# Kernel tuning notes

Hardware: AMD Instinct MI355X
Metric: run time of the kernel (lower is better)

The kernel has to match this reference:

```python
import jax, jax.numpy as jnp
import numpy as np
import math

N_HEADS = 8

def _head_dirs():
    # 8 trigrams = corners of {-1,+1}^3, L2-normalized -> each row / sqrt(3)
    t = np.array([[ (i >> 2 & 1) * 2 - 1, (i >> 1 & 1) * 2 - 1, (i & 1) * 2 - 1]
                  for i in range(8)], dtype=np.float32)
    return jnp.asarray(t / np.sqrt(3.0, dtype=np.float32))

def setup_inputs() -> dict:
    key = jax.random.key(0)
    k1, k2, k3, k4 = jax.random.split(key, 4)
    B, T, C = 2, 2048, 1024
    x = jax.random.normal(k1, (B, T, C), dtype=jnp.float32)
    w_qkv = jax.random.normal(k2, (C, 3 * C), dtype=jnp.float32) * (1.0 / math.sqrt(C))
    w_out = jax.random.normal(k3, (C, C), dtype=jnp.float32) * (1.0 / math.sqrt(C))
    head_scales = jax.random.normal(k4, (N_HEADS,), dtype=jnp.float32) * 0.1
    return {"x": x, "w_qkv": w_qkv, "w_out": w_out, "head_scales": head_scales}

def reference(x, w_qkv, w_out, head_scales):
    B, T, C = x.shape
    H = N_HEADS
    hd = C // H
    scale = 1.0 / math.sqrt(hd)
    dirs = _head_dirs()  # [H,3], fixed buffer

    qkv = (x @ w_qkv).reshape(B, T, 3, H, hd)
    q = jnp.transpose(qkv[:, :, 0], (0, 2, 1, 3))  # [B,H,T,hd]
    k = jnp.transpose(qkv[:, :, 1], (0, 2, 1, 3))
    v = jnp.transpose(qkv[:, :, 2], (0, 2, 1, 3))

    scores = jnp.einsum('bhqd,bhkd->bhqk', q, k) * scale  # [B,H,T,T]
    causal = jnp.tril(jnp.ones((T, T), dtype=bool))
    scores = jnp.where(causal[None, None], scores, -jnp.inf)

    # rank-1 geometric (trigram) bias on first 3 dims of q,k
    q_proj = jnp.einsum('bhtd,hd->bht', q[..., :3], dirs)  # [B,H,T]
    k_proj = jnp.einsum('bhtd,hd->bht', k[..., :3], dirs)
    geo = q_proj[..., :, None] * k_proj[..., None, :]       # [B,H,T,T]
    scores = scores + head_scales[None, :, None, None] * geo

    attn = jax.nn.softmax(scores, axis=-1)
    out = jnp.einsum('bhqk,bhkd->bqhd', attn, v).reshape(B, T, C)
    return out @ w_out
```

## Files before the change

kernel.cpp:

```cpp
#include <hip/hip_runtime.h>
#include <hip/hip_bf16.h>
#include <cstdint>
#include <cstddef>


namespace {
constexpr int kB = 2, kT = 2048, kC = 1024, kHD = 128;
constexpr int kM = kB * kT;
constexpr int kN3 = 3 * kC;
constexpr float kScale = 0.08838834764831845f;
constexpr float kInvS3 = 0.57735026918962576f;
constexpr float kL2E  = 1.4426950408889634f;
}

typedef __bf16 bf16x8 __attribute__((ext_vector_type(8)));
typedef float f32x4 __attribute__((ext_vector_type(4)));
typedef unsigned short u16x8 __attribute__((ext_vector_type(8)));
typedef unsigned short u16x4 __attribute__((ext_vector_type(4)));
typedef unsigned int u32x4 __attribute__((ext_vector_type(4)));

__device__ __forceinline__ unsigned short f2b(float f) {
  return __builtin_bit_cast(unsigned short, (__bf16)f);
}
__device__ __forceinline__ float b2f(unsigned short u) {
  return (float)__builtin_bit_cast(__bf16, u);
}
__device__ __forceinline__ void gll16(const void* g, void* lds) {
  __builtin_amdgcn_global_load_lds(
      (const __attribute__((address_space(1))) unsigned int*)g,
      (__attribute__((address_space(3))) unsigned int*)lds, 16, 0, 0);
}
__device__ __forceinline__ bf16x8 ldsv(const unsigned short* p) {
  return __builtin_bit_cast(bf16x8, *(const u16x8*)p);
}
__device__ __forceinline__ uint2 tr16(const unsigned short* p) {
  uint2 r;
  unsigned off = (unsigned)(uintptr_t)(const __attribute__((address_space(3))) unsigned short*)p;
  asm volatile("ds_read_b64_tr_b16 %0, %1" : "=v"(r) : "v"(off));
  return r;
}

__device__ __forceinline__ void tc_body(const float* __restrict__ in,
                                        unsigned short* __restrict__ out,
                                        int R, int Cin, int bx, int by, int t) {
  __shared__ float tile[64][65];
  const int r0 = by * 64, c0 = bx * 64;
  const int tr = t >> 4, tc4 = (t & 15) * 4;
#pragma unroll
  for (int rr = 0; rr < 4; ++rr) {
    int r = tr + rr * 16;
    float4 v = *(const float4*)&in[(size_t)(r0 + r) * Cin + c0 + tc4];
    tile[r][tc4 + 0] = v.x; tile[r][tc4 + 1] = v.y;
    tile[r][tc4 + 2] = v.z; tile[r][tc4 + 3] = v.w;
  }
  __syncthreads();
#pragma unroll
  for (int rr = 0; rr < 4; ++rr) {
    int c = tr + rr * 16;
    u16x4 o = { f2b(tile[tc4 + 0][c]), f2b(tile[tc4 + 1][c]),
                f2b(tile[tc4 + 2][c]), f2b(tile[tc4 + 3][c]) };
    *(u16x4*)&out[(size_t)(c0 + c) * R + r0 + tc4] = o;
  }
}

__global__ void k_prep(const float* __restrict__ x, unsigned short* __restrict__ xb,
                       const float* __restrict__ wqkv, unsigned short* __restrict__ wqkvT) {
  const int bid = (int)blockIdx.x;
  const int t = threadIdx.x;
  if (bid < 4096) {
    int i = bid * 256 + t;
    float4 v = ((const float4*)x)[i];
    u16x4 o = { f2b(v.x), f2b(v.y), f2b(v.z), f2b(v.w) };
    ((u16x4*)xb)[i] = o;
  } else {
    int r = bid - 4096;
    tc_body(wqkv, wqkvT, kC, kN3, r % 48, r / 48, t);
  }
}

__global__ __launch_bounds__(256, 2) void k_gemm(
    const unsigned short* __restrict__ A,
    const unsigned short* __restrict__ Bt,
    unsigned short* __restrict__ Cb,
    float* __restrict__ Cf,
    int M, int N, int K, int ldc) {
  __shared__ unsigned short sA[2][4096];
  __shared__ unsigned short sB[2][4096];
  const int t = threadIdx.x;
  const int lane = t & 63, wave = t >> 6;
  const int g = lane >> 4, c16 = lane & 15;
  const int wr = wave >> 1, wc = wave & 1;
  const int brow = blockIdx.x * 128, bcol = blockIdx.y * 128;
  const int NT = K >> 5;

  f32x4 acc[4][4];
#pragma unroll
  for (int m = 0; m < 4; ++m)
#pragma unroll
    for (int n = 0; n < 4; ++n) acc[m][n] = 0.f;

  auto stage = [&](int buf, int kt) {
    const int k0 = kt * 32;
#pragma unroll
    for (int is = 0; is < 2; ++is) {
      int row = is * 64 + (t >> 2);
      int gs = (t & 3) ^ (row & 3);
      gll16(&A[(size_t)(brow + row) * K + k0 + gs * 8], &sA[buf][is * 2048 + wave * 512]);
      gll16(&Bt[(size_t)(bcol + row) * K + k0 + gs * 8], &sB[buf][is * 2048 + wave * 512]);
    }
  };

  stage(0, 0);
  __syncthreads();
  for (int kt = 0; kt < NT; ++kt) {
    if (kt + 1 < NT) stage((kt + 1) & 1, kt + 1);
    const int buf = kt & 1;
    bf16x8 av[4], bv[4];
#pragma unroll
    for (int m = 0; m < 4; ++m) {
      int row = wr * 64 + m * 16 + c16;
      av[m] = ldsv(&sA[buf][row * 32 + (g ^ (row & 3)) * 8]);
    }
#pragma unroll
    for (int n = 0; n < 4; ++n) {
      int row = wc * 64 + n * 16 + c16;
      bv[n] = ldsv(&sB[buf][row * 32 + (g ^ (row & 3)) * 8]);
    }
    __builtin_amdgcn_s_setprio(1);
#pragma unroll
    for (int m = 0; m < 4; ++m)
#pragma unroll
      for (int n = 0; n < 4; ++n)
        acc[m][n] = __builtin_amdgcn_mfma_f32_16x16x32_bf16(av[m], bv[n], acc[m][n], 0, 0, 0);
    __builtin_amdgcn_s_setprio(0);
    __syncthreads();
  }

  const int orow = brow + wr * 64, ocol = bcol + wc * 64;
  if (Cb != nullptr) {
#pragma unroll
    for (int m = 0; m < 4; ++m)
#pragma unroll
      for (int n = 0; n < 4; ++n)
#pragma unroll
        for (int jj = 0; jj < 4; ++jj)
          Cb[(size_t)(orow + m * 16 + g * 4 + jj) * ldc + ocol + n * 16 + c16] =
              f2b(acc[m][n][jj]);
  } else {
#pragma unroll
    for (int m = 0; m < 4; ++m)
#pragma unroll
      for (int n = 0; n < 4; ++n)
#pragma unroll
        for (int jj = 0; jj < 4; ++jj)
          Cf[(size_t)(orow + m * 16 + g * 4 + jj) * ldc + ocol + n * 16 + c16] =
              acc[m][n][jj];
  }
}

__constant__ unsigned char kItem[44] = {
  60, 61,
  62, 56, 57, 58, 52,
  53, 54, 48, 49,
  50, 44, 45, 46, 40,
  41, 42, 36, 37,
  38, 32, 33, 34, 28,
  29, 30, 24, 25,
  26, 20, 21, 22, 16,
  17, 18, 12, 13, 8, 9,
  14, 4, 5, 0 };

__global__ __launch_bounds__(256, 2) void k_attn(
    const unsigned short* __restrict__ qkv,
    const float* __restrict__ head_scales,
    unsigned short* __restrict__ pO0,
    unsigned short* __restrict__ pO1,
    unsigned short* __restrict__ pO2,
    float2* __restrict__ pml) {
  __shared__ unsigned short sK[8192];
  __shared__ unsigned short sV[2][8192];
  __shared__ float sKp[2][64];

  const int t = threadIdx.x;
  const int lane = t & 63, wave = t >> 6;
  const int g = lane >> 4, c16 = lane & 15;
  const int bh = blockIdx.x;
  const int it = kItem[blockIdx.y];
  const int qt = it >> 2, c = it & 3;
  const int n = 2 * qt + 2;
  const int nc = (qt == 0) ? 1 : (qt <= 2) ? 2 : 3;
  const int cbase = n / nc, crem = n % nc;
  const int t0 = c * cbase + (c < crem ? c : crem);
  const int t1 = t0 + cbase + (c < crem ? 1 : 0);

  const int b = bh >> 3, h = bh & 7;
  const float hs = head_scales[h];
  const float sx = (h & 4) ? 1.f : -1.f;
  const float sy = (h & 2) ? 1.f : -1.f;
  const float sz = (h & 1) ? 1.f : -1.f;

  const int q0w = qt * 128 + wave * 32;
  const size_t rowbase = (size_t)b * kT;

  bf16x8 aq[2][4];
  float qp[2];
#pragma unroll
  for (int m = 0; m < 2; ++m) {
    const unsigned short* qrow = &qkv[(rowbase + q0w + m * 16 + c16) * kN3 + h * kHD];
#pragma unroll
    for (int ks = 0; ks < 4; ++ks) aq[m][ks] = ldsv(qrow + ks * 32 + g * 8);
    qp[m] = hs * kInvS3 * (sx * b2f(qrow[0]) + sy * b2f(qrow[1]) + sz * b2f(qrow[2]));
  }

  float mrow[2] = { -__builtin_inff(), -__builtin_inff() };
  float lrow[2] = { 0.f, 0.f };
  f32x4 oacc[2][8];
#pragma unroll
  for (int m = 0; m < 2; ++m)
#pragma unroll
    for (int dn = 0; dn < 8; ++dn) oacc[m][dn] = 0.f;

  uint2 kpr;

  auto stageK = [&](int jt) {
    const int j0 = jt * 64;
#pragma unroll
    for (int is = 0; is < 4; ++is) {
      int row = is * 16 + (t >> 4);
      int gp = t & 15;
      int gs = (gp & 8) | ((gp ^ (row & 7)) & 7);
      gll16(&qkv[(rowbase + j0 + row) * kN3 + kC + h * kHD + gs * 8],
            &sK[is * 2048 + wave * 512]);
    }
  };
  auto stageV = [&](int jt, int buf) {
    const int j0 = jt * 64;
    const int vrow = ((lane >> 3) << 2) + ((lane >> 1) & 3);
    const int vcol = (lane & 1) * 8;
#pragma unroll
    for (int d = 0; d < 2; ++d) {
      const int dn = wave * 2 + d;
#pragma unroll
      for (int hf2 = 0; hf2 < 2; ++hf2) {
        gll16(&qkv[(rowbase + j0 + hf2 * 32 + vrow) * kN3 + 2 * kC + h * kHD
                   + dn * 16 + vcol],
              &sV[buf][dn * 1024 + hf2 * 512]);
      }
    }
  };
  auto loadKp = [&](int jt) {
    if (wave == 0)
      kpr = *(const uint2*)&qkv[(rowbase + jt * 64 + lane) * kN3 + kC + h * kHD];
  };
  auto writeKp = [&](int buf) {
    if (wave == 0) {
      float e0 = b2f((unsigned short)(kpr.x & 0xffffu));
      float e1 = b2f((unsigned short)(kpr.x >> 16));
      float e2 = b2f((unsigned short)(kpr.y & 0xffffu));
      sKp[buf][lane] = kInvS3 * (sx * e0 + sy * e1 + sz * e2);
    }
  };

  stageK(t0); stageV(t0, 0); loadKp(t0);
  writeKp(0);
  __syncthreads();

  for (int jt = t0; jt < t1; ++jt) {
    const int vbuf = (jt - t0) & 1;
    const bool more = (jt + 1 < t1);
    const int j0 = jt * 64;

    f32x4 s[2][4];
#pragma unroll
    for (int m = 0; m < 2; ++m)
#pragma unroll
      for (int nn = 0; nn < 4; ++nn) s[m][nn] = 0.f;
#pragma unroll
    for (int ks = 0; ks < 4; ++ks) {
      bf16x8 kb[4];
#pragma unroll
      for (int nn = 0; nn < 4; ++nn) {
        int gp = ks * 4 + g;
        int gp2 = (gp & 8) | ((gp ^ (c16 & 7)) & 7);
        kb[nn] = ldsv(&sK[(nn * 16 + c16) * 128 + gp2 * 8]);
      }
      __builtin_amdgcn_s_setprio(1);
#pragma unroll
      for (int m = 0; m < 2; ++m)
#pragma unroll
        for (int nn = 0; nn < 4; ++nn)
          s[m][nn] = __builtin_amdgcn_mfma_f32_16x16x32_bf16(kb[nn], aq[m][ks], s[m][nn], 0, 0, 0);
      __builtin_amdgcn_s_setprio(0);
    }

    __syncthreads();
    if (more) { stageK(jt + 1); stageV(jt + 1, vbuf ^ 1); loadKp(jt + 1); }

    float kpv[4][4];
#pragma unroll
    for (int nn = 0; nn < 4; ++nn)
#pragma unroll
      for (int jj = 0; jj < 4; ++jj) kpv[nn][jj] = sKp[vbuf][nn * 16 + g * 4 + jj];

    const bool edge = (jt >= 2 * qt);
    unsigned int paf[2][2][4];
#pragma unroll
    for (int m = 0; m < 2; ++m) {
      const int qg = q0w + m * 16 + c16;
      float vmax = -__builtin_inff();
#pragma unroll
      for (int nn = 0; nn < 4; ++nn)
#pragma unroll
        for (int jj = 0; jj < 4; ++jj) {
          float xv = s[m][nn][jj] * kScale + qp[m] * kpv[nn][jj];
          if (edge) {
            int kvg = j0 + nn * 16 + g * 4 + jj;
            xv = (kvg <= qg) ? xv : -__builtin_inff();
          }
          s[m][nn][jj] = xv;
          vmax = fmaxf(vmax, xv);
        }
      vmax = fmaxf(vmax, __shfl_xor(vmax, 16, 64));
      vmax = fmaxf(vmax, __shfl_xor(vmax, 32, 64));

      if (__any(vmax > mrow[m] + 8.f)) {
        float mnew = fmaxf(mrow[m], vmax);
        float mc0 = fmaxf(mnew, -1e30f);
        float alpha = exp2f((mrow[m] - mc0) * kL2E);
        mrow[m] = mnew;
        lrow[m] *= alpha;
        float ao[4];
#pragma unroll
        for (int jj = 0; jj < 4; ++jj)
          ao[jj] = __shfl(alpha, (lane & 48) | (g * 4 + jj), 64);
#pragma unroll
        for (int dn = 0; dn < 8; ++dn)
#pragma unroll
          for (int jj = 0; jj < 4; ++jj) oacc[m][dn][jj] *= ao[jj];
      }

      unsigned int pk[4][2];
      {
        const float mc = fmaxf(mrow[m], -1e30f);
        float ls = 0.f;
#pragma unroll
        for (int nn = 0; nn < 4; ++nn) {
          float p0 = exp2f((s[m][nn][0] - mc) * kL2E);
          float p1 = exp2f((s[m][nn][1] - mc) * kL2E);
          float p2 = exp2f((s[m][nn][2] - mc) * kL2E);
          float p3 = exp2f((s[m][nn][3] - mc) * kL2E);
          ls += (p0 + p1) + (p2 + p3);
          pk[nn][0] = (unsigned)f2b(p0) | ((unsigned)f2b(p1) << 16);
          pk[nn][1] = (unsigned)f2b(p2) | ((unsigned)f2b(p3) << 16);
        }
        lrow[m] += ls;
      }
#pragma unroll
      for (int ks2 = 0; ks2 < 2; ++ks2)
#pragma unroll
        for (int w = 0; w < 4; ++w) {
          int src = c16 + (((lane >> 4) & 1) * 2 + (w >> 1)) * 16;
          int va  = __shfl((int)pk[2 * ks2][w & 1], src, 64);
          int vb_ = __shfl((int)pk[2 * ks2 + 1][w & 1], src, 64);
          paf[m][ks2][w] = (unsigned)((lane & 32) ? vb_ : va);
        }
    }

#pragma unroll
    for (int ks2 = 0; ks2 < 2; ++ks2) {
      bf16x8 pa0 = __builtin_bit_cast(bf16x8,
          (u32x4){paf[0][ks2][0], paf[0][ks2][1], paf[0][ks2][2], paf[0][ks2][3]});
      bf16x8 pa1 = __builtin_bit_cast(bf16x8,
          (u32x4){paf[1][ks2][0], paf[1][ks2][1], paf[1][ks2][2], paf[1][ks2][3]});
      uint2 trv[8][2];
#pragma unroll
      for (int dn = 0; dn < 8; ++dn)
#pragma unroll
        for (int hf = 0; hf < 2; ++hf)
          trv[dn][hf] = tr16(&sV[vbuf][dn * 1024 + (ks2 * 8 + 2 * g + hf) * 64 + c16 * 4]);
      asm volatile("s_waitcnt lgkmcnt(0)" ::: "memory");
      __builtin_amdgcn_sched_barrier(0);
      __builtin_amdgcn_s_setprio(1);
#pragma unroll
      for (int dn = 0; dn < 8; ++dn) {
        bf16x8 vb = __builtin_bit_cast(bf16x8,
            (u32x4){trv[dn][0].x, trv[dn][0].y, trv[dn][1].x, trv[dn][1].y});
        oacc[0][dn] = __builtin_amdgcn_mfma_f32_16x16x32_bf16(pa0, vb, oacc[0][dn], 0, 0, 0);
        oacc[1][dn] = __builtin_amdgcn_mfma_f32_16x16x32_bf16(pa1, vb, oacc[1][dn], 0, 0, 0);
      }
      __builtin_amdgcn_s_setprio(0);
    }

    if (more) {
      writeKp(vbuf ^ 1);
      __syncthreads();
    }
  }

  unsigned short* pout = (c == 0) ? pO0 : (c == 1) ? pO1 : pO2;
#pragma unroll
  for (int m = 0; m < 2; ++m) {
    float lt = lrow[m];
    lt += __shfl_xor(lt, 16, 64);
    lt += __shfl_xor(lt, 32, 64);
    if (g == 0) {
      int rowi = wave * 32 + m * 16 + c16;
      pml[c * 32768 + (bh * 16 + qt) * 128 + rowi] = make_float2(mrow[m], lt);
    }
#pragma unroll
    for (int dn = 0; dn < 8; ++dn)
#pragma unroll
      for (int jj = 0; jj < 4; ++jj) {
        int r = q0w + m * 16 + g * 4 + jj;
        pout[(rowbase + r) * kC + h * kHD + dn * 16 + c16] = f2b(oacc[m][dn][jj]);
      }
  }
}

__global__ void k_fin(unsigned short* __restrict__ p0,
                      const unsigned short* __restrict__ p1,
                      const unsigned short* __restrict__ p2,
                      const float2* __restrict__ pml,
                      const float* __restrict__ wout,
                      unsigned short* __restrict__ woutT) {
  const int bid = (int)blockIdx.x;
  const int t = threadIdx.x;
  if (bid >= 256) {
    int r = bid - 256;
    tc_body(wout, woutT, kC, kC, r & 15, r >> 4, t);
    return;
  }
  const int bh = bid & 15, qt = bid >> 4;
  const int row = t >> 1, half = t & 1;
  const int b = bh >> 3, h = bh & 7;
  const size_t base = ((size_t)b * kT + qt * 128 + row) * kC + h * kHD + half * 64;
  const int nc = (qt == 0) ? 1 : (qt <= 2) ? 2 : 3;
  const int mli = (bh * 16 + qt) * 128 + row;
  float2 ml0 = pml[mli];
  float2 ml1 = make_float2(-1e30f, 0.f), ml2 = make_float2(-1e30f, 0.f);
  float mm = ml0.x;
  if (nc > 1) { ml1 = pml[32768 + mli]; mm = fmaxf(mm, ml1.x); }
  if (nc > 2) { ml2 = pml[65536 + mli]; mm = fmaxf(mm, ml2.x); }
  const float w0 = exp2f((ml0.x - mm) * kL2E);
  const float w1 = (nc > 1) ? exp2f((ml1.x - mm) * kL2E) : 0.f;
  const float w2 = (nc > 2) ? exp2f((ml2.x - mm) * kL2E) : 0.f;
  const float inv = 1.0f / (w0 * ml0.y + w1 * ml1.y + w2 * ml2.y);
#pragma unroll
  for (int i = 0; i < 8; ++i) {
    u16x8 o0 = *(const u16x8*)&p0[base + i * 8];
    u16x8 r;
    if (nc == 1) {
#pragma unroll
      for (int j = 0; j < 8; ++j) r[j] = f2b(b2f(o0[j]) * inv);
    } else if (nc == 2) {
      u16x8 o1 = *(const u16x8*)&p1[base + i * 8];
#pragma unroll
      for (int j = 0; j < 8; ++j)
        r[j] = f2b((w0 * b2f(o0[j]) + w1 * b2f(o1[j])) * inv);
    } else {
      u16x8 o1 = *(const u16x8*)&p1[base + i * 8];
      u16x8 o2 = *(const u16x8*)&p2[base + i * 8];
#pragma unroll
      for (int j = 0; j < 8; ++j)
        r[j] = f2b((w0 * b2f(o0[j]) + w1 * b2f(o1[j]) + w2 * b2f(o2[j])) * inv);
    }
    *(u16x8*)&p0[base + i * 8] = r;
  }
}

extern "C" void kernel_launch(void* const* d_in, const int* in_sizes, int n_in,
                              void* d_out, int out_size, void* d_ws, size_t ws_size,
                              hipStream_t stream) {
  const float* x    = (const float*)d_in[0];
  const float* wqkv = (const float*)d_in[1];
  const float* wout = (const float*)d_in[2];
  const float* hsc  = (const float*)d_in[3];
  char* ws = (char*)d_ws;
  unsigned short* xb    = (unsigned short*)(ws);
  unsigned short* wqkvT = (unsigned short*)(ws + 8388608);
  unsigned short* qkvb  = (unsigned short*)(ws + 16777216);
  unsigned short* attnb = (unsigned short*)(ws + 41943040);
  unsigned short* woutT = (unsigned short*)(ws + 16777216);
  float2* pml = (float2*)d_out;
  float* out = (float*)d_out;

  k_prep<<<dim3(4864), dim3(256), 0, stream>>>(x, xb, wqkv, wqkvT);
  k_gemm<<<dim3(32, 24), dim3(256), 0, stream>>>(xb, wqkvT, qkvb, nullptr, kM, kN3, kC, kN3);
  k_attn<<<dim3(16, 44), dim3(256), 0, stream>>>(qkvb, hsc, attnb, xb, wqkvT, pml);
  k_fin<<<dim3(512), dim3(256), 0, stream>>>(attnb, xb, wqkvT, pml, wout, woutT);
  k_gemm<<<dim3(32, 8), dim3(256), 0, stream>>>(attnb, woutT, nullptr, out, kM, kC, kC, kC);
}
```

Before: 128.8 us.

## Split attention block into 8 waves of 16 query rows each

Moves the attention kernel from 4 waves handling 32 query rows each to 8 waves handling 16 rows each. This halves per-wave accumulator and score registers and spreads K/V staging across more threads. The aim is more waves in flight per CU to hide latency. In exchange, each wave now reads the shared K and V tiles for only half as many rows, so LDS traffic per MFMA doubles and the larger block synchronises more waves.

```diff
diff --git a/kernel.cpp b/kernel.cpp
--- a/kernel.cpp
+++ b/kernel.cpp
@@ -170,7 +170,7 @@
   17, 18, 12, 13, 8, 9,
   14, 4, 5, 0 };
 
-__global__ __launch_bounds__(256, 2) void k_attn(
+__global__ __launch_bounds__(512, 2) void k_attn(
     const unsigned short* __restrict__ qkv,
     const float* __restrict__ head_scales,
     unsigned short* __restrict__ pO0,
@@ -199,53 +199,44 @@
   const float sy = (h & 2) ? 1.f : -1.f;
   const float sz = (h & 1) ? 1.f : -1.f;
 
-  const int q0w = qt * 128 + wave * 32;
+  const int q0w = qt * 128 + wave * 16;
   const size_t rowbase = (size_t)b * kT;
 
-  bf16x8 aq[2][4];
-  float qp[2];
-#pragma unroll
-  for (int m = 0; m < 2; ++m) {
-    const unsigned short* qrow = &qkv[(rowbase + q0w + m * 16 + c16) * kN3 + h * kHD];
-#pragma unroll
-    for (int ks = 0; ks < 4; ++ks) aq[m][ks] = ldsv(qrow + ks * 32 + g * 8);
-    qp[m] = hs * kInvS3 * (sx * b2f(qrow[0]) + sy * b2f(qrow[1]) + sz * b2f(qrow[2]));
-  }
-
-  float mrow[2] = { -__builtin_inff(), -__builtin_inff() };
-  float lrow[2] = { 0.f, 0.f };
-  f32x4 oacc[2][8];
-#pragma unroll
-  for (int m = 0; m < 2; ++m)
-#pragma unroll
-    for (int dn = 0; dn < 8; ++dn) oacc[m][dn] = 0.f;
+  bf16x8 aq[4];
+  const unsigned short* qrow = &qkv[(rowbase + q0w + c16) * kN3 + h * kHD];
+#pragma unroll
+  for (int ks = 0; ks < 4; ++ks) aq[ks] = ldsv(qrow + ks * 32 + g * 8);
+  const float qp = hs * kInvS3 * (sx * b2f(qrow[0]) + sy * b2f(qrow[1]) + sz * b2f(qrow[2]));
+
+  float mrow = -__builtin_inff();
+  float lrow = 0.f;
+  f32x4 oacc[8];
+#pragma unroll
+  for (int dn = 0; dn < 8; ++dn) oacc[dn] = 0.f;
 
   uint2 kpr;
 
   auto stageK = [&](int jt) {
     const int j0 = jt * 64;
 #pragma unroll
-    for (int is = 0; is < 4; ++is) {
-      int row = is * 16 + (t >> 4);
+    for (int is = 0; is < 2; ++is) {
+      int row = is * 32 + (t >> 4);
       int gp = t & 15;
       int gs = (gp & 8) | ((gp ^ (row & 7)) & 7);
       gll16(&qkv[(rowbase + j0 + row) * kN3 + kC + h * kHD + gs * 8],
-            &sK[is * 2048 + wave * 512]);
+            &sK[is * 4096 + wave * 512]);
     }
   };
   auto stageV = [&](int jt, int buf) {
     const int j0 = jt * 64;
     const int vrow = ((lane >> 3) << 2) + ((lane >> 1) & 3);
     const int vcol = (lane & 1) * 8;
-#pragma unroll
-    for (int d = 0; d < 2; ++d) {
-      const int dn = wave * 2 + d;
-#pragma unroll
-      for (int hf2 = 0; hf2 < 2; ++hf2) {
-        gll16(&qkv[(rowbase + j0 + hf2 * 32 + vrow) * kN3 + 2 * kC + h * kHD
-                   + dn * 16 + vcol],
-              &sV[buf][dn * 1024 + hf2 * 512]);
-      }
+    const int dn = wave;
+#pragma unroll
+    for (int hf2 = 0; hf2 < 2; ++hf2) {
+      gll16(&qkv[(rowbase + j0 + hf2 * 32 + vrow) * kN3 + 2 * kC + h * kHD
+                 + dn * 16 + vcol],
+            &sV[buf][dn * 1024 + hf2 * 512]);
     }
   };
   auto loadKp = [&](int jt) {
@@ -270,11 +261,9 @@
     const bool more = (jt + 1 < t1);
     const int j0 = jt * 64;
 
-    f32x4 s[2][4];
-#pragma unroll
-    for (int m = 0; m < 2; ++m)
-#pragma unroll
-      for (int nn = 0; nn < 4; ++nn) s[m][nn] = 0.f;
+    f32x4 s[4];
+#pragma unroll
+    for (int nn = 0; nn < 4; ++nn) s[nn] = 0.f;
 #pragma unroll
     for (int ks = 0; ks < 4; ++ks) {
       bf16x8 kb[4];
@@ -286,10 +275,8 @@
       }
       __builtin_amdgcn_s_setprio(1);
 #pragma unroll
-      for (int m = 0; m < 2; ++m)
-#pragma unroll
-        for (int nn = 0; nn < 4; ++nn)
-          s[m][nn] = __builtin_amdgcn_mfma_f32_16x16x32_bf16(kb[nn], aq[m][ks], s[m][nn], 0, 0, 0);
+      for (int nn = 0; nn < 4; ++nn)
+        s[nn] = __builtin_amdgcn_mfma_f32_16x16x32_bf16(kb[nn], aq[ks], s[nn], 0, 0, 0);
       __builtin_amdgcn_s_setprio(0);
     }
 
@@ -303,32 +290,31 @@
       for (int jj = 0; jj < 4; ++jj) kpv[nn][jj] = sKp[vbuf][nn * 16 + g * 4 + jj];
 
     const bool edge = (jt >= 2 * qt);
-    unsigned int paf[2][2][4];
-#pragma unroll
-    for (int m = 0; m < 2; ++m) {
-      const int qg = q0w + m * 16 + c16;
+    unsigned int paf[2][4];
+    {
+      const int qg = q0w + c16;
       float vmax = -__builtin_inff();
 #pragma unroll
       for (int nn = 0; nn < 4; ++nn)
 #pragma unroll
         for (int jj = 0; jj < 4; ++jj) {
-          float xv = s[m][nn][jj] * kScale + qp[m] * kpv[nn][jj];
+          float xv = s[nn][jj] * kScale + qp * kpv[nn][jj];
           if (edge) {
             int kvg = j0 + nn * 16 + g * 4 + jj;
             xv = (kvg <= qg) ? xv : -__builtin_inff();
           }
-          s[m][nn][jj] = xv;
+          s[nn][jj] = xv;
           vmax = fmaxf(vmax, xv);
         }
       vmax = fmaxf(vmax, __shfl_xor(vmax, 16, 64));
       vmax = fmaxf(vmax, __shfl_xor(vmax, 32, 64));
 
-      if (__any(vmax > mrow[m] + 8.f)) {
-        float mnew = fmaxf(mrow[m], vmax);
+      if (__any(vmax > mrow + 8.f)) {
+        float mnew = fmaxf(mrow, vmax);
         float mc0 = fmaxf(mnew, -1e30f);
-        float alpha = exp2f((mrow[m] - mc0) * kL2E);
-        mrow[m] = mnew;
-        lrow[m] *= alpha;
+        float alpha = exp2f((mrow - mc0) * kL2E);
+        mrow = mnew;
+        lrow *= alpha;
         float ao[4];
 #pragma unroll
         for (int jj = 0; jj < 4; ++jj)
@@ -336,24 +322,24 @@
 #pragma unroll
         for (int dn = 0; dn < 8; ++dn)
 #pragma unroll
-          for (int jj = 0; jj < 4; ++jj) oacc[m][dn][jj] *= ao[jj];
+          for (int jj = 0; jj < 4; ++jj) oacc[dn][jj] *= ao[jj];
       }
 
       unsigned int pk[4][2];
       {
-        const float mc = fmaxf(mrow[m], -1e30f);
+        const float mc = fmaxf(mrow, -1e30f);
         float ls = 0.f;
 #pragma unroll
         for (int nn = 0; nn < 4; ++nn) {
-          float p0 = exp2f((s[m][nn][0] - mc) * kL2E);
-          float p1 = exp2f((s[m][nn][1] - mc) * kL2E);
-          float p2 = exp2f((s[m][nn][2] - mc) * kL2E);
-          float p3 = exp2f((s[m][nn][3] - mc) * kL2E);
+          float p0 = exp2f((s[nn][0] - mc) * kL2E);
+          float p1 = exp2f((s[nn][1] - mc) * kL2E);
+          float p2 = exp2f((s[nn][2] - mc) * kL2E);
+          float p3 = exp2f((s[nn][3] - mc) * kL2E);
           ls += (p0 + p1) + (p2 + p3);
           pk[nn][0] = (unsigned)f2b(p0) | ((unsigned)f2b(p1) << 16);
           pk[nn][1] = (unsigned)f2b(p2) | ((unsigned)f2b(p3) << 16);
         }
-        lrow[m] += ls;
+        lrow += ls;
       }
 #pragma unroll
       for (int ks2 = 0; ks2 < 2; ++ks2)
@@ -362,16 +348,14 @@
           int src = c16 + (((lane >> 4) & 1) * 2 + (w >> 1)) * 16;
           int va  = __shfl((int)pk[2 * ks2][w & 1], src, 64);
           int vb_ = __shfl((int)pk[2 * ks2 + 1][w & 1], src, 64);
-          paf[m][ks2][w] = (unsigned)((lane & 32) ? vb_ : va);
+          paf[ks2][w] = (unsigned)((lane & 32) ? vb_ : va);
         }
     }
 
 #pragma unroll
     for (int ks2 = 0; ks2 < 2; ++ks2) {
-      bf16x8 pa0 = __builtin_bit_cast(bf16x8,
-          (u32x4){paf[0][ks2][0], paf[0][ks2][1], paf[0][ks2][2], paf[0][ks2][3]});
-      bf16x8 pa1 = __builtin_bit_cast(bf16x8,
-          (u32x4){paf[1][ks2][0], paf[1][ks2][1], paf[1][ks2][2], paf[1][ks2][3]});
+      bf16x8 pa = __builtin_bit_cast(bf16x8,
+          (u32x4){paf[ks2][0], paf[ks2][1], paf[ks2][2], paf[ks2][3]});
       uint2 trv[8][2];
 #pragma unroll
       for (int dn = 0; dn < 8; ++dn)
@@ -385,8 +369,7 @@
       for (int dn = 0; dn < 8; ++dn) {
         bf16x8 vb = __builtin_bit_cast(bf16x8,
             (u32x4){trv[dn][0].x, trv[dn][0].y, trv[dn][1].x, trv[dn][1].y});
-        oacc[0][dn] = __builtin_amdgcn_mfma_f32_16x16x32_bf16(pa0, vb, oacc[0][dn], 0, 0, 0);
-        oacc[1][dn] = __builtin_amdgcn_mfma_f32_16x16x32_bf16(pa1, vb, oacc[1][dn], 0, 0, 0);
+        oacc[dn] = __builtin_amdgcn_mfma_f32_16x16x32_bf16(pa, vb, oacc[dn], 0, 0, 0);
       }
       __builtin_amdgcn_s_setprio(0);
     }
@@ -398,21 +381,20 @@
   }
 
   unsigned short* pout = (c == 0) ? pO0 : (c == 1) ? pO1 : pO2;
-#pragma unroll
-  for (int m = 0; m < 2; ++m) {
-    float lt = lrow[m];
+  {
+    float lt = lrow;
     lt += __shfl_xor(lt, 16, 64);
     lt += __shfl_xor(lt, 32, 64);
     if (g == 0) {
-      int rowi = wave * 32 + m * 16 + c16;
-      pml[c * 32768 + (bh * 16 + qt) * 128 + rowi] = make_float2(mrow[m], lt);
+      int rowi = wave * 16 + c16;
+      pml[c * 32768 + (bh * 16 + qt) * 128 + rowi] = make_float2(mrow, lt);
     }
 #pragma unroll
     for (int dn = 0; dn < 8; ++dn)
 #pragma unroll
       for (int jj = 0; jj < 4; ++jj) {
-        int r = q0w + m * 16 + g * 4 + jj;
-        pout[(rowbase + r) * kC + h * kHD + dn * 16 + c16] = f2b(oacc[m][dn][jj]);
+        int r = q0w + g * 4 + jj;
+        pout[(rowbase + r) * kC + h * kHD + dn * 16 + c16] = f2b(oacc[dn][jj]);
       }
   }
 }
@@ -486,7 +468,7 @@
 
   k_prep<<<dim3(4864), dim3(256), 0, stream>>>(x, xb, wqkv, wqkvT);
   k_gemm<<<dim3(32, 24), dim3(256), 0, stream>>>(xb, wqkvT, qkvb, nullptr, kM, kN3, kC, kN3);
-  k_attn<<<dim3(16, 44), dim3(256), 0, stream>>>(qkvb, hsc, attnb, xb, wqkvT, pml);
+  k_attn<<<dim3(16, 44), dim3(512), 0, stream>>>(qkvb, hsc, attnb, xb, wqkvT, pml);
   k_fin<<<dim3(512), dim3(256), 0, stream>>>(attnb, xb, wqkvT, pml, wout, woutT);
   k_gemm<<<dim3(32, 8), dim3(256), 0, stream>>>(attnb, woutT, nullptr, out, kM, kC, kC, kC);
 }
```

Result: slower. 138.6 us (+7.6%).
